# Kernel tuning notes

Hardware: AMD Instinct MI355X
Metric: run time of the kernel (lower is better)

## Reference

```python
import jax, jax.numpy as jnp
import numpy as np

N_NODES = 50000


def _sage_layer(x, edges, W_neigh, W_self, b):
    """HeteroGraphConv(sum) of per-relation DGL SAGEConv(mean).

    x:        [N, F_in] node features (single node type)
    edges:    [R, 2, E] int (src, dst) per relation
    W_neigh:  [R, F_in, F_out], W_self: [R, F_in, F_out], b: [R, F_out]
    returns:  [N, F_out]
    """
    N = x.shape[0]
    R = edges.shape[0]
    out = jnp.zeros((N, W_neigh.shape[-1]), dtype=x.dtype)
    for r in range(R):  # small fixed number of relation types
        src = edges[r, 0]
        dst = edges[r, 1]
        # mean-aggregate neighbor features onto dst
        s = jax.ops.segment_sum(x[src], dst, num_segments=N)          # [N, F_in]
        deg = jax.ops.segment_sum(jnp.ones_like(dst, dtype=x.dtype), dst,
                                  num_segments=N)                     # [N]
        mean = s / jnp.maximum(deg, 1.0)[:, None]                     # zero-deg -> 0
        # SAGEConv(mean): fc_self(h_dst) + fc_neigh(mean_neigh) + bias
        out = out + x @ W_self[r] + mean @ W_neigh[r] + b[r]
    return out


def setup_inputs() -> dict:
    key = jax.random.key(0)
    ks = jax.random.split(key, 10)
    F_in, H, O, R, E = 128, 128, 64, 2, 800000
    scale_in = 1.0 / np.sqrt(F_in)
    scale_h = 1.0 / np.sqrt(H)
    return {
        "x": jax.random.normal(ks[0], (N_NODES, F_in), dtype=jnp.float32),
        "edges": jax.random.randint(ks[1], (R, 2, E), 0, N_NODES, dtype=jnp.int32),
        "neg_edges": jax.random.randint(ks[2], (2, E), 0, N_NODES, dtype=jnp.int32),
        "W_neigh1": jax.random.normal(ks[3], (R, F_in, H), jnp.float32) * scale_in,
        "W_self1": jax.random.normal(ks[4], (R, F_in, H), jnp.float32) * scale_in,
        "b1": jnp.zeros((R, H), jnp.float32),
        "W_neigh2": jax.random.normal(ks[5], (R, H, O), jnp.float32) * scale_h,
        "W_self2": jax.random.normal(ks[6], (R, H, O), jnp.float32) * scale_h,
        "b2": jnp.zeros((R, O), jnp.float32),
    }


def reference(x, edges, neg_edges, W_neigh1, W_self1, b1, W_neigh2, W_self2, b2):
    h = _sage_layer(x, edges, W_neigh1, W_self1, b1)
    h = jax.nn.relu(h)
    h = _sage_layer(h, edges, W_neigh2, W_self2, b2)          # [N, O]
    # HeteroDotProductPredictor: u_dot_v on edges of the scored etype (rel 0)
    pos_score = jnp.sum(h[edges[0, 0]] * h[edges[0, 1]], axis=-1)      # [E]
    neg_score = jnp.sum(h[neg_edges[0]] * h[neg_edges[1]], axis=-1)    # [E_neg]
    return pos_score, neg_score
```

## Files before the change

### kernel.cpp

```cpp
#include <hip/hip_runtime.h>


#define BW 128
#define NBK_MAX 1024
#define EPB 8192

typedef __attribute__((ext_vector_type(8))) short bf16x8;
typedef __attribute__((ext_vector_type(4))) float floatx4;

__device__ __forceinline__ unsigned short f2bf(float f) {
    unsigned u = __float_as_uint(f);
    unsigned r = u + 0x7FFFu + ((u >> 16) & 1u);
    return (unsigned short)(r >> 16);
}
__device__ __forceinline__ unsigned pack2(float a, float b) {
    return (unsigned)f2bf(a) | ((unsigned)f2bf(b) << 16);
}
__device__ __forceinline__ float bflo(unsigned v) { return __uint_as_float(v << 16); }
__device__ __forceinline__ float bfhi(unsigned v) { return __uint_as_float(v & 0xFFFF0000u); }

__global__ __launch_bounds__(256) void
bucket_count_kernel(const int* __restrict__ edges, int* __restrict__ bcnt,
                    int NBK, int E)
{
    __shared__ int cnt[2 * NBK_MAX];
    const int rbT = 2 * NBK;
    const int t = threadIdx.x;
    for (int k = t; k < rbT; k += 256) cnt[k] = 0;
    __syncthreads();
    long long start = (long long)blockIdx.x * EPB;
    long long twoE = 2LL * E;
    for (int u = 0; u < EPB / 256; ++u) {
        long long idx = start + u * 256 + t;
        if (idx < twoE) {
            int r = idx >= E;
            int e = (int)(idx - (long long)r * E);
            int d = edges[(size_t)r * 2 * E + E + e];
            atomicAdd(&cnt[r * NBK + (d >> 7)], 1);
        }
    }
    __syncthreads();
    for (int k = t; k < rbT; k += 256)
        if (cnt[k]) atomicAdd(&bcnt[k], cnt[k]);
}

__global__ __launch_bounds__(1024) void
bucket_scan_kernel(const int* __restrict__ bcnt, int* __restrict__ bko,
                   int rbT, int twoE)
{
    __shared__ int sm[1024];
    int t = threadIdx.x;
    int v = (t < rbT) ? bcnt[t] : 0;
    sm[t] = v;
    __syncthreads();
    for (int s = 1; s < 1024; s <<= 1) {
        int u = (t >= s) ? sm[t - s] : 0;
        __syncthreads();
        sm[t] += u;
        __syncthreads();
    }
    if (t < rbT) bko[t] = sm[t] - v;
    if (t == 0) bko[rbT] = twoE;
}

__global__ __launch_bounds__(256) void
partition_kernel(const int* __restrict__ edges, const int* __restrict__ bko,
                 int* __restrict__ gcur, uint2* __restrict__ staging,
                 int NBK, int E)
{
    __shared__ int cnt[2 * NBK_MAX];
    __shared__ int base[2 * NBK_MAX];
    const int rbT = 2 * NBK;
    const int t = threadIdx.x;
    for (int k = t; k < rbT; k += 256) cnt[k] = 0;
    __syncthreads();
    long long start = (long long)blockIdx.x * EPB;
    long long twoE = 2LL * E;
    for (int u = 0; u < EPB / 256; ++u) {
        long long idx = start + u * 256 + t;
        if (idx < twoE) {
            int r = idx >= E;
            int e = (int)(idx - (long long)r * E);
            int d = edges[(size_t)r * 2 * E + E + e];
            atomicAdd(&cnt[r * NBK + (d >> 7)], 1);
        }
    }
    __syncthreads();
    for (int k = t; k < rbT; k += 256) {
        int c0 = cnt[k];
        if (c0) base[k] = bko[k] + atomicAdd(&gcur[k], c0);
        cnt[k] = 0;
    }
    __syncthreads();
    for (int u = 0; u < EPB / 256; ++u) {
        long long idx = start + u * 256 + t;
        if (idx < twoE) {
            int r = idx >= E;
            int e = (int)(idx - (long long)r * E);
            int s = edges[(size_t)r * 2 * E + e];
            int d = edges[(size_t)r * 2 * E + E + e];
            int rb = r * NBK + (d >> 7);
            int pos = atomicAdd(&cnt[rb], 1);
            staging[(size_t)base[rb] + pos] = make_uint2((unsigned)s, (unsigned)d);
        }
    }
}

__global__ __launch_bounds__(256) void
bucket_csr_kernel(const uint2* __restrict__ staging, const int* __restrict__ bko,
                  int* __restrict__ csr, int* __restrict__ off,
                  int NBK, int N)
{
    __shared__ int hist[BW], excl[BW], cur[BW], sc[BW];
    const int rb = blockIdx.x;
    const int r = rb / NBK;
    const int b = rb % NBK;
    const int node0 = b * BW;
    const int nn = min(BW, N - node0);
    const int cbase = bko[rb];
    const int c = bko[rb + 1] - cbase;
    const int t = threadIdx.x;

    if (t < BW) { hist[t] = 0; cur[t] = 0; }
    __syncthreads();
    for (int k = t; k < c; k += 256)
        atomicAdd(&hist[(int)staging[(size_t)cbase + k].y - node0], 1);
    __syncthreads();
    if (t < BW) sc[t] = hist[t];
    __syncthreads();
    for (int s = 1; s < BW; s <<= 1) {
        int v = (t < BW && t >= s) ? sc[t - s] : 0;
        __syncthreads();
        if (t < BW) sc[t] += v;
        __syncthreads();
    }
    if (t < BW) excl[t] = sc[t] - hist[t];
    if (t < nn) off[(size_t)r * N + node0 + t] = cbase + excl[t];
    __syncthreads();
    for (int k = t; k < c; k += 256) {
        uint2 pr = staging[(size_t)cbase + k];
        int l = (int)pr.y - node0;
        int pos = atomicAdd(&cur[l], 1);
        csr[(size_t)cbase + excl[l] + pos] = (int)pr.x;
    }
}

__global__ void cvt_kernel(const float* __restrict__ in,
                           unsigned short* __restrict__ o, int n4)
{
    int t = blockIdx.x * blockDim.x + threadIdx.x;
    if (t >= n4) return;
    float4 v = ((const float4*)in)[t];
    ushort4 r;
    r.x = f2bf(v.x); r.y = f2bf(v.y); r.z = f2bf(v.z); r.w = f2bf(v.w);
    ((ushort4*)o)[t] = r;
}

__global__ void prep_kernel(const float* __restrict__ Ws1, const float* __restrict__ Wn1,
                            const float* __restrict__ b1,
                            const float* __restrict__ Ws2, const float* __restrict__ Wn2,
                            const float* __restrict__ b2,
                            unsigned short* __restrict__ WT1z, unsigned short* __restrict__ WT1a,
                            unsigned short* __restrict__ WT1b, float* __restrict__ bc1,
                            unsigned short* __restrict__ WT2z, unsigned short* __restrict__ WT2a,
                            unsigned short* __restrict__ WT2b, float* __restrict__ bc2)
{
    int t = blockIdx.x * blockDim.x + threadIdx.x;
    if (t < 16384) {
        int n = t >> 7, k = t & 127;
        int in = k * 128 + n;
        WT1z[t] = f2bf(Ws1[in] + Ws1[16384 + in]);
        WT1a[t] = f2bf(Wn1[in]);
        WT1b[t] = f2bf(Wn1[16384 + in]);
    }
    if (t < 8192) {
        int n = t >> 7, k = t & 127;
        int in = k * 64 + n;
        WT2z[t] = f2bf(Ws2[in] + Ws2[8192 + in]);
        WT2a[t] = f2bf(Wn2[in]);
        WT2b[t] = f2bf(Wn2[8192 + in]);
    }
    if (t < 128) bc1[t] = b1[t] + b1[128 + t];
    if (t < 64)  bc2[t] = b2[t] + b2[64 + t];
}

__global__ __launch_bounds__(256) void
agg1_kernel(const unsigned short* __restrict__ xb,
            const int* __restrict__ csr, const int* __restrict__ off,
            unsigned short* __restrict__ m0, unsigned short* __restrict__ m1,
            int N, int twoE)
{
    int w = blockIdx.x * 4 + (threadIdx.x >> 6);
    int lane = threadIdx.x & 63;
    if (w >= N) return;
    const int col = lane * 2;

    float sx0 = 0.f, sy0 = 0.f, sx1 = 0.f, sy1 = 0.f;
    int o0 = __builtin_amdgcn_readfirstlane(off[w]);
    int o1 = __builtin_amdgcn_readfirstlane(off[w + 1]);
    int d0 = o1 - o0;
    int j = o0;
    for (; j + 7 < o1; j += 8) {
        int s0 = __builtin_amdgcn_readfirstlane(csr[j]);
        int s1 = __builtin_amdgcn_readfirstlane(csr[j + 1]);
        int s2 = __builtin_amdgcn_readfirstlane(csr[j + 2]);
        int s3 = __builtin_amdgcn_readfirstlane(csr[j + 3]);
        int s4 = __builtin_amdgcn_readfirstlane(csr[j + 4]);
        int s5 = __builtin_amdgcn_readfirstlane(csr[j + 5]);
        int s6 = __builtin_amdgcn_readfirstlane(csr[j + 6]);
        int s7 = __builtin_amdgcn_readfirstlane(csr[j + 7]);
        unsigned a0 = *(const unsigned*)(xb + (size_t)s0 * 128 + col);
        unsigned a1 = *(const unsigned*)(xb + (size_t)s1 * 128 + col);
        unsigned a2 = *(const unsigned*)(xb + (size_t)s2 * 128 + col);
        unsigned a3 = *(const unsigned*)(xb + (size_t)s3 * 128 + col);
        unsigned a4 = *(const unsigned*)(xb + (size_t)s4 * 128 + col);
        unsigned a5 = *(const unsigned*)(xb + (size_t)s5 * 128 + col);
        unsigned a6 = *(const unsigned*)(xb + (size_t)s6 * 128 + col);
        unsigned a7 = *(const unsigned*)(xb + (size_t)s7 * 128 + col);
        sx0 += ((bflo(a0) + bflo(a1)) + (bflo(a2) + bflo(a3))) +
               ((bflo(a4) + bflo(a5)) + (bflo(a6) + bflo(a7)));
        sy0 += ((bfhi(a0) + bfhi(a1)) + (bfhi(a2) + bfhi(a3))) +
               ((bfhi(a4) + bfhi(a5)) + (bfhi(a6) + bfhi(a7)));
    }
    for (; j < o1; ++j) {
        int s0 = __builtin_amdgcn_readfirstlane(csr[j]);
        unsigned a = *(const unsigned*)(xb + (size_t)s0 * 128 + col);
        sx0 += bflo(a); sy0 += bfhi(a);
    }
    int p = N + w;
    o0 = __builtin_amdgcn_readfirstlane(off[p]);
    o1 = (p + 1 < 2 * N) ? __builtin_amdgcn_readfirstlane(off[p + 1]) : twoE;
    int d1 = o1 - o0;
    j = o0;
    for (; j + 7 < o1; j += 8) {
        int s0 = __builtin_amdgcn_readfirstlane(csr[j]);
        int s1 = __builtin_amdgcn_readfirstlane(csr[j + 1]);
        int s2 = __builtin_amdgcn_readfirstlane(csr[j + 2]);
        int s3 = __builtin_amdgcn_readfirstlane(csr[j + 3]);
        int s4 = __builtin_amdgcn_readfirstlane(csr[j + 4]);
        int s5 = __builtin_amdgcn_readfirstlane(csr[j + 5]);
        int s6 = __builtin_amdgcn_readfirstlane(csr[j + 6]);
        int s7 = __builtin_amdgcn_readfirstlane(csr[j + 7]);
        unsigned a0 = *(const unsigned*)(xb + (size_t)s0 * 128 + col);
        unsigned a1 = *(const unsigned*)(xb + (size_t)s1 * 128 + col);
        unsigned a2 = *(const unsigned*)(xb + (size_t)s2 * 128 + col);
        unsigned a3 = *(const unsigned*)(xb + (size_t)s3 * 128 + col);
        unsigned a4 = *(const unsigned*)(xb + (size_t)s4 * 128 + col);
        unsigned a5 = *(const unsigned*)(xb + (size_t)s5 * 128 + col);
        unsigned a6 = *(const unsigned*)(xb + (size_t)s6 * 128 + col);
        unsigned a7 = *(const unsigned*)(xb + (size_t)s7 * 128 + col);
        sx1 += ((bflo(a0) + bflo(a1)) + (bflo(a2) + bflo(a3))) +
               ((bflo(a4) + bflo(a5)) + (bflo(a6) + bflo(a7)));
        sy1 += ((bfhi(a0) + bfhi(a1)) + (bfhi(a2) + bfhi(a3))) +
               ((bfhi(a4) + bfhi(a5)) + (bfhi(a6) + bfhi(a7)));
    }
    for (; j < o1; ++j) {
        int s0 = __builtin_amdgcn_readfirstlane(csr[j]);
        unsigned a = *(const unsigned*)(xb + (size_t)s0 * 128 + col);
        sx1 += bflo(a); sy1 += bfhi(a);
    }
    float inv0 = 1.0f / fmaxf((float)d0, 1.0f);
    float inv1 = 1.0f / fmaxf((float)d1, 1.0f);
    *(unsigned*)(m0 + (size_t)w * 128 + col) = pack2(sx0 * inv0, sy0 * inv0);
    *(unsigned*)(m1 + (size_t)w * 128 + col) = pack2(sx1 * inv1, sy1 * inv1);
}

__global__ __launch_bounds__(256) void
gemm1_fused_kernel(const unsigned short* __restrict__ xb,
                   const unsigned short* __restrict__ m0,
                   const unsigned short* __restrict__ m1,
                   const unsigned short* __restrict__ WTz,
                   const unsigned short* __restrict__ WTa,
                   const unsigned short* __restrict__ WTb,
                   const float* __restrict__ bias,
                   unsigned short* __restrict__ h1b, int N)
{
    __shared__ float eb[64][129];

    const int tid = threadIdx.x;
    const int wave = tid >> 6;
    const int lane = tid & 63;
    const int m = lane & 15;
    const int quad = lane >> 4;

    floatx4 acc[8];
    const floatx4 z4 = {0.f, 0.f, 0.f, 0.f};
#pragma unroll
    for (int t = 0; t < 8; ++t) acc[t] = z4;

    int arow = blockIdx.x * 64 + wave * 16 + m;
    if (arow >= N) arow = N - 1;
    const size_t abase = (size_t)arow * 128 + quad * 8;

#pragma unroll
    for (int s = 0; s < 4; ++s) {
        bf16x8 ax = *(const bf16x8*)(xb + abase + s * 32);
        bf16x8 a0 = *(const bf16x8*)(m0 + abase + s * 32);
        bf16x8 a1 = *(const bf16x8*)(m1 + abase + s * 32);
#pragma unroll
        for (int t = 0; t < 8; ++t) {
            const size_t bo = (size_t)(t * 16 + m) * 128 + s * 32 + quad * 8;
            acc[t] = __builtin_amdgcn_mfma_f32_16x16x32_bf16(
                ax, *(const bf16x8*)(WTz + bo), acc[t], 0, 0, 0);
            acc[t] = __builtin_amdgcn_mfma_f32_16x16x32_bf16(
                a0, *(const bf16x8*)(WTa + bo), acc[t], 0, 0, 0);
            acc[t] = __builtin_amdgcn_mfma_f32_16x16x32_bf16(
                a1, *(const bf16x8*)(WTb + bo), acc[t], 0, 0, 0);
        }
    }

#pragma unroll
    for (int t = 0; t < 8; ++t)
#pragma unroll
        for (int i = 0; i < 4; ++i)
            eb[wave * 16 + quad * 4 + i][t * 16 + m] = acc[t][i];
    __syncthreads();

#pragma unroll
    for (int j = 0; j < 4; ++j) {
        int lr = wave * 16 + j * 4 + quad;
        int grow = blockIdx.x * 64 + lr;
        if (grow < N) {
#pragma unroll
            for (int i = 0; i < 2; ++i) {
                int c0 = (i * 16 + m) * 4;
                float v0 = fmaxf(eb[lr][c0 + 0] + bias[c0 + 0], 0.0f);
                float v1 = fmaxf(eb[lr][c0 + 1] + bias[c0 + 1], 0.0f);
                float v2 = fmaxf(eb[lr][c0 + 2] + bias[c0 + 2], 0.0f);
                float v3 = fmaxf(eb[lr][c0 + 3] + bias[c0 + 3], 0.0f);
                ushort4 u;
                u.x = f2bf(v0); u.y = f2bf(v1); u.z = f2bf(v2); u.w = f2bf(v3);
                *(ushort4*)(h1b + (size_t)grow * 128 + c0) = u;
            }
        }
    }
}

template<int BN>
__global__ __launch_bounds__(256) void
gemm_mfma_kernel(const unsigned short* __restrict__ Ab,
                 const unsigned short* __restrict__ WTz,
                 const unsigned short* __restrict__ WTa,
                 const unsigned short* __restrict__ WTb,
                 const float* __restrict__ bias,
                 float* __restrict__ zf,
                 unsigned short* __restrict__ ya, unsigned short* __restrict__ yb,
                 int N)
{
    constexpr int NT = BN / 16;
    __shared__ float eb[64][BN + 1];

    const int tid = threadIdx.x;
    const int wave = tid >> 6;
    const int lane = tid & 63;
    const int m = lane & 15;
    const int quad = lane >> 4;
    const int sel = blockIdx.y;
    const unsigned short* WT = (sel == 0) ? WTz : ((sel == 1) ? WTa : WTb);

    floatx4 acc[NT];
    const floatx4 z4 = {0.f, 0.f, 0.f, 0.f};
#pragma unroll
    for (int t = 0; t < NT; ++t) acc[t] = z4;

    int arow = blockIdx.x * 64 + wave * 16 + m;
    if (arow >= N) arow = N - 1;
    const unsigned short* aptr = Ab + (size_t)arow * 128 + quad * 8;

#pragma unroll
    for (int s = 0; s < 4; ++s) {
        bf16x8 a = *(const bf16x8*)(aptr + s * 32);
#pragma unroll
        for (int t = 0; t < NT; ++t) {
            bf16x8 b = *(const bf16x8*)(WT + (size_t)(t * 16 + m) * 128 + s * 32 + quad * 8);
            acc[t] = __builtin_amdgcn_mfma_f32_16x16x32_bf16(a, b, acc[t], 0, 0, 0);
        }
    }

#pragma unroll
    for (int t = 0; t < NT; ++t)
#pragma unroll
        for (int i = 0; i < 4; ++i)
            eb[wave * 16 + quad * 4 + i][t * 16 + m] = acc[t][i];
    __syncthreads();

#pragma unroll
    for (int j = 0; j < 4; ++j) {
        int lr = wave * 16 + j * 4 + quad;
        int grow = blockIdx.x * 64 + lr;
        if (grow < N) {
#pragma unroll
            for (int i = 0; i < BN / 64; ++i) {
                int c0 = (i * 16 + m) * 4;
                float v0 = eb[lr][c0 + 0], v1 = eb[lr][c0 + 1];
                float v2 = eb[lr][c0 + 2], v3 = eb[lr][c0 + 3];
                if (sel == 0) {
                    float4 o;
                    o.x = v0 + bias[c0 + 0];
                    o.y = v1 + bias[c0 + 1];
                    o.z = v2 + bias[c0 + 2];
                    o.w = v3 + bias[c0 + 3];
                    *(float4*)(zf + (size_t)grow * BN + c0) = o;
                } else {
                    unsigned short* ob = (sel == 1) ? ya : yb;
                    ushort4 u;
                    u.x = f2bf(v0); u.y = f2bf(v1); u.z = f2bf(v2); u.w = f2bf(v3);
                    *(ushort4*)(ob + (size_t)grow * BN + c0) = u;
                }
            }
        }
    }
}

__global__ __launch_bounds__(256) void
agg2_kernel(const unsigned short* __restrict__ t0,
            const unsigned short* __restrict__ t1,
            const float* __restrict__ z2,
            const int* __restrict__ csr, const int* __restrict__ off,
            unsigned short* __restrict__ h2b, int N, int twoE)
{
    int w = blockIdx.x * 4 + (threadIdx.x >> 6);
    int lane = threadIdx.x & 63;
    if (w >= N) return;
    const int half = lane >> 5;
    const int col = (lane & 31) * 2;

    float sx0 = 0.f, sy0 = 0.f, sx1 = 0.f, sy1 = 0.f;
    int o0 = __builtin_amdgcn_readfirstlane(off[w]);
    int o1 = __builtin_amdgcn_readfirstlane(off[w + 1]);
    int d0 = o1 - o0;
    int j = o0 + half;
    for (; j + 6 < o1; j += 8) {
        int s0 = csr[j], s1 = csr[j + 2], s2 = csr[j + 4], s3 = csr[j + 6];
        unsigned a0 = *(const unsigned*)(t0 + (size_t)s0 * 64 + col);
        unsigned a1 = *(const unsigned*)(t0 + (size_t)s1 * 64 + col);
        unsigned a2 = *(const unsigned*)(t0 + (size_t)s2 * 64 + col);
        unsigned a3 = *(const unsigned*)(t0 + (size_t)s3 * 64 + col);
        sx0 += (bflo(a0) + bflo(a1)) + (bflo(a2) + bflo(a3));
        sy0 += (bfhi(a0) + bfhi(a1)) + (bfhi(a2) + bfhi(a3));
    }
    for (; j < o1; j += 2) {
        unsigned a = *(const unsigned*)(t0 + (size_t)csr[j] * 64 + col);
        sx0 += bflo(a); sy0 += bfhi(a);
    }
    int p = N + w;
    o0 = __builtin_amdgcn_readfirstlane(off[p]);
    o1 = (p + 1 < 2 * N) ? __builtin_amdgcn_readfirstlane(off[p + 1]) : twoE;
    int d1 = o1 - o0;
    j = o0 + half;
    for (; j + 6 < o1; j += 8) {
        int s0 = csr[j], s1 = csr[j + 2], s2 = csr[j + 4], s3 = csr[j + 6];
        unsigned a0 = *(const unsigned*)(t1 + (size_t)s0 * 64 + col);
        unsigned a1 = *(const unsigned*)(t1 + (size_t)s1 * 64 + col);
        unsigned a2 = *(const unsigned*)(t1 + (size_t)s2 * 64 + col);
        unsigned a3 = *(const unsigned*)(t1 + (size_t)s3 * 64 + col);
        sx1 += (bflo(a0) + bflo(a1)) + (bflo(a2) + bflo(a3));
        sy1 += (bfhi(a0) + bfhi(a1)) + (bfhi(a2) + bfhi(a3));
    }
    for (; j < o1; j += 2) {
        unsigned a = *(const unsigned*)(t1 + (size_t)csr[j] * 64 + col);
        sx1 += bflo(a); sy1 += bfhi(a);
    }
    sx0 += __shfl_xor(sx0, 32);
    sy0 += __shfl_xor(sy0, 32);
    sx1 += __shfl_xor(sx1, 32);
    sy1 += __shfl_xor(sy1, 32);
    if (half == 0) {
        float inv0 = 1.0f / fmaxf((float)d0, 1.0f);
        float inv1 = 1.0f / fmaxf((float)d1, 1.0f);
        float2 z = *(const float2*)(z2 + (size_t)w * 64 + col);
        float hx = z.x + sx0 * inv0 + sx1 * inv1;
        float hy = z.y + sy0 * inv0 + sy1 * inv1;
        *(unsigned*)(h2b + (size_t)w * 64 + col) = pack2(hx, hy);
    }
}

__global__ __launch_bounds__(256) void
score_kernel(const unsigned short* __restrict__ h,
             const int* __restrict__ edges, const int* __restrict__ neg,
             float* __restrict__ out, int E, int En)
{
    int t = blockIdx.x * blockDim.x + threadIdx.x;
    int e = t >> 3;
    int c = t & 7;
    if (e >= E + En) return;
    int sI, dI, oI;
    if (e < E) { sI = edges[e]; dI = edges[E + e]; oI = e; }
    else { int en = e - E; sI = neg[en]; dI = neg[En + en]; oI = E + en; }
    uint4 va = *(const uint4*)(h + (size_t)sI * 64 + c * 8);
    uint4 vb = *(const uint4*)(h + (size_t)dI * 64 + c * 8);
    float s = 0.0f;
    s = fmaf(bflo(va.x), bflo(vb.x), s);
    s = fmaf(bfhi(va.x), bfhi(vb.x), s);
    s = fmaf(bflo(va.y), bflo(vb.y), s);
    s = fmaf(bfhi(va.y), bfhi(vb.y), s);
    s = fmaf(bflo(va.z), bflo(vb.z), s);
    s = fmaf(bfhi(va.z), bfhi(vb.z), s);
    s = fmaf(bflo(va.w), bflo(vb.w), s);
    s = fmaf(bfhi(va.w), bfhi(vb.w), s);
    s += __shfl_xor(s, 1);
    s += __shfl_xor(s, 2);
    s += __shfl_xor(s, 4);
    if (c == 0) out[oI] = s;
}

extern "C" void kernel_launch(void* const* d_in, const int* in_sizes, int n_in,
                              void* d_out, int out_size, void* d_ws, size_t ws_size,
                              hipStream_t stream)
{
    const float* x     = (const float*)d_in[0];
    const int*   edges = (const int*)d_in[1];
    const int*   neg   = (const int*)d_in[2];
    const float* Wn1   = (const float*)d_in[3];
    const float* Ws1   = (const float*)d_in[4];
    const float* b1    = (const float*)d_in[5];
    const float* Wn2   = (const float*)d_in[6];
    const float* Ws2   = (const float*)d_in[7];
    const float* b2    = (const float*)d_in[8];
    float* out = (float*)d_out;

    const int Fin = 128, R = 2;
    const int N  = in_sizes[0] / Fin;
    const int E  = in_sizes[1] / (R * 2);
    const int En = in_sizes[2] / 2;
    const int twoE = 2 * E;
    const int NBK = (N + BW - 1) / BW;
    const int rbT = 2 * NBK;

    const size_t nb128 = (size_t)N * 128 * sizeof(unsigned short);
    char* p = (char*)d_ws;

    uint2* staging = (uint2*)p;
    float* z2      = (float*)p;
    {
        size_t r0 = (size_t)twoE * sizeof(uint2);
        size_t r1 = (size_t)N * 64 * sizeof(float);
        p += (r0 > r1 ? r0 : r1);
    }
    unsigned short* m0  = (unsigned short*)p; p += nb128;
    unsigned short* m1  = (unsigned short*)p; p += nb128;
    unsigned short* xb  = (unsigned short*)p; p += nb128;
    unsigned short* h1b = (unsigned short*)p; p += nb128;
    unsigned short* WT1z = (unsigned short*)p; p += 16384 * 2;
    unsigned short* WT1a = (unsigned short*)p; p += 16384 * 2;
    unsigned short* WT1b = (unsigned short*)p; p += 16384 * 2;
    unsigned short* WT2z = (unsigned short*)p; p += 8192 * 2;
    unsigned short* WT2a = (unsigned short*)p; p += 8192 * 2;
    unsigned short* WT2b = (unsigned short*)p; p += 8192 * 2;
    float* bc1 = (float*)p; p += 128 * sizeof(float);
    float* bc2 = (float*)p; p += 64 * sizeof(float);
    int* bcnt = (int*)p; p += (size_t)2 * NBK_MAX * sizeof(int);
    int* gcur = (int*)p; p += (size_t)2 * NBK_MAX * sizeof(int);
    int* bko  = (int*)p; p += ((size_t)2 * NBK_MAX + 1) * sizeof(int);
    int* off  = (int*)p; p += (size_t)2 * N * sizeof(int);
    int* csr  = (int*)p;

    unsigned short* t0  = m0;
    unsigned short* t1  = m0 + (size_t)N * 64;
    unsigned short* h2b = m1;

    const int BS = 256;
    const int edge_blocks = (twoE + EPB - 1) / EPB;
    const int gx = (N + 63) / 64;

    hipMemsetAsync(bcnt, 0, (size_t)4 * NBK_MAX * sizeof(int), stream);
    bucket_count_kernel<<<edge_blocks, BS, 0, stream>>>(edges, bcnt, NBK, E);
    bucket_scan_kernel<<<1, 1024, 0, stream>>>(bcnt, bko, rbT, twoE);
    partition_kernel<<<edge_blocks, BS, 0, stream>>>(edges, bko, gcur, staging, NBK, E);
    bucket_csr_kernel<<<rbT, BS, 0, stream>>>(staging, bko, csr, off, NBK, N);

    cvt_kernel<<<(N * 32 + BS - 1) / BS, BS, 0, stream>>>(x, xb, N * 32);
    prep_kernel<<<(16384 + BS - 1) / BS, BS, 0, stream>>>(
        Ws1, Wn1, b1, Ws2, Wn2, b2,
        WT1z, WT1a, WT1b, bc1, WT2z, WT2a, WT2b, bc2);

    agg1_kernel<<<(N + 3) / 4, BS, 0, stream>>>(xb, csr, off, m0, m1, N, twoE);
    gemm1_fused_kernel<<<gx, BS, 0, stream>>>(xb, m0, m1, WT1z, WT1a, WT1b,
                                              bc1, h1b, N);

    {
        dim3 g(gx, 3);
        gemm_mfma_kernel<64><<<g, BS, 0, stream>>>(h1b, WT2z, WT2a, WT2b, bc2,
                                                   z2, t0, t1, N);
    }
    agg2_kernel<<<(N + 3) / 4, BS, 0, stream>>>(t0, t1, z2, csr, off, h2b, N, twoE);

    score_kernel<<<((E + En) * 8 + BS - 1) / BS, BS, 0, stream>>>(
        h2b, edges, neg, out, E, En);
}
```

Before: 383.7 us.

## Split gather rows across half-waves with wider loads; fuse layer-2 GEMM outputs

agg1 now has each half-wave gather a different neighbor row with 8-byte loads, merging the halves by shuffle. agg2 now uses quarter-wave groups of four rows each with 8-byte loads. Both aim to put more independent memory requests in flight per wave. The three-way blockIdx.y layer-2 GEMM is merged into one kernel that reloads the A tile once and computes all three outputs, at the cost of more accumulator registers and extra shared-memory round trips.

```diff
diff --git a/kernel.cpp b/kernel.cpp
--- a/kernel.cpp
+++ b/kernel.cpp
@@ -18,6 +18,7 @@
 }
 __device__ __forceinline__ float bflo(unsigned v) { return __uint_as_float(v << 16); }
 __device__ __forceinline__ float bfhi(unsigned v) { return __uint_as_float(v & 0xFFFF0000u); }
+#define RFL(x) __builtin_amdgcn_readfirstlane(x)
 
 __global__ __launch_bounds__(256) void
 bucket_count_kernel(const int* __restrict__ edges, int* __restrict__ bcnt,
@@ -193,76 +194,119 @@
     int w = blockIdx.x * 4 + (threadIdx.x >> 6);
     int lane = threadIdx.x & 63;
     if (w >= N) return;
-    const int col = lane * 2;
-
-    float sx0 = 0.f, sy0 = 0.f, sx1 = 0.f, sy1 = 0.f;
-    int o0 = __builtin_amdgcn_readfirstlane(off[w]);
-    int o1 = __builtin_amdgcn_readfirstlane(off[w + 1]);
+    const int half = lane >> 5;
+    const int col = (lane & 31) * 4;
+    const unsigned short* xc = xb + col;
+
+    float a0 = 0.f, a1 = 0.f, a2 = 0.f, a3 = 0.f;
+    float b0 = 0.f, b1 = 0.f, b2 = 0.f, b3 = 0.f;
+
+    int o0 = RFL(off[w]);
+    int o1 = RFL(off[w + 1]);
     int d0 = o1 - o0;
     int j = o0;
+    for (; j + 15 < o1; j += 16) {
+        int cc[16];
+#pragma unroll
+        for (int k = 0; k < 16; ++k) cc[k] = RFL(csr[j + k]);
+#pragma unroll
+        for (int k = 0; k < 8; ++k) {
+            int row = half ? cc[2 * k + 1] : cc[2 * k];
+            uint2 v = *(const uint2*)(xc + (size_t)row * 128);
+            a0 += bflo(v.x); a1 += bfhi(v.x);
+            a2 += bflo(v.y); a3 += bfhi(v.y);
+        }
+    }
     for (; j + 7 < o1; j += 8) {
-        int s0 = __builtin_amdgcn_readfirstlane(csr[j]);
-        int s1 = __builtin_amdgcn_readfirstlane(csr[j + 1]);
-        int s2 = __builtin_amdgcn_readfirstlane(csr[j + 2]);
-        int s3 = __builtin_amdgcn_readfirstlane(csr[j + 3]);
-        int s4 = __builtin_amdgcn_readfirstlane(csr[j + 4]);
-        int s5 = __builtin_amdgcn_readfirstlane(csr[j + 5]);
-        int s6 = __builtin_amdgcn_readfirstlane(csr[j + 6]);
-        int s7 = __builtin_amdgcn_readfirstlane(csr[j + 7]);
-        unsigned a0 = *(const unsigned*)(xb + (size_t)s0 * 128 + col);
-        unsigned a1 = *(const unsigned*)(xb + (size_t)s1 * 128 + col);
-        unsigned a2 = *(const unsigned*)(xb + (size_t)s2 * 128 + col);
-        unsigned a3 = *(const unsigned*)(xb + (size_t)s3 * 128 + col);
-        unsigned a4 = *(const unsigned*)(xb + (size_t)s4 * 128 + col);
-        unsigned a5 = *(const unsigned*)(xb + (size_t)s5 * 128 + col);
-        unsigned a6 = *(const unsigned*)(xb + (size_t)s6 * 128 + col);
-        unsigned a7 = *(const unsigned*)(xb + (size_t)s7 * 128 + col);
-        sx0 += ((bflo(a0) + bflo(a1)) + (bflo(a2) + bflo(a3))) +
-               ((bflo(a4) + bflo(a5)) + (bflo(a6) + bflo(a7)));
-        sy0 += ((bfhi(a0) + bfhi(a1)) + (bfhi(a2) + bfhi(a3))) +
-               ((bfhi(a4) + bfhi(a5)) + (bfhi(a6) + bfhi(a7)));
-    }
-    for (; j < o1; ++j) {
-        int s0 = __builtin_amdgcn_readfirstlane(csr[j]);
-        unsigned a = *(const unsigned*)(xb + (size_t)s0 * 128 + col);
-        sx0 += bflo(a); sy0 += bfhi(a);
-    }
+        int cc[8];
+#pragma unroll
+        for (int k = 0; k < 8; ++k) cc[k] = RFL(csr[j + k]);
+#pragma unroll
+        for (int k = 0; k < 4; ++k) {
+            int row = half ? cc[2 * k + 1] : cc[2 * k];
+            uint2 v = *(const uint2*)(xc + (size_t)row * 128);
+            a0 += bflo(v.x); a1 += bfhi(v.x);
+            a2 += bflo(v.y); a3 += bfhi(v.y);
+        }
+    }
+    for (; j + 1 < o1; j += 2) {
+        int rlo = RFL(csr[j]);
+        int rhi = RFL(csr[j + 1]);
+        int row = half ? rhi : rlo;
+        uint2 v = *(const uint2*)(xc + (size_t)row * 128);
+        a0 += bflo(v.x); a1 += bfhi(v.x);
+        a2 += bflo(v.y); a3 += bfhi(v.y);
+    }
+    if (j < o1) {
+        int row = RFL(csr[j]);
+        if (half == 0) {
+            uint2 v = *(const uint2*)(xc + (size_t)row * 128);
+            a0 += bflo(v.x); a1 += bfhi(v.x);
+            a2 += bflo(v.y); a3 += bfhi(v.y);
+        }
+    }
+
     int p = N + w;
-    o0 = __builtin_amdgcn_readfirstlane(off[p]);
-    o1 = (p + 1 < 2 * N) ? __builtin_amdgcn_readfirstlane(off[p + 1]) : twoE;
+    o0 = RFL(off[p]);
+    o1 = (p + 1 < 2 * N) ? RFL(off[p + 1]) : twoE;
     int d1 = o1 - o0;
     j = o0;
+    for (; j + 15 < o1; j += 16) {
+        int cc[16];
+#pragma unroll
+        for (int k = 0; k < 16; ++k) cc[k] = RFL(csr[j + k]);
+#pragma unroll
+        for (int k = 0; k < 8; ++k) {
+            int row = half ? cc[2 * k + 1] : cc[2 * k];
+            uint2 v = *(const uint2*)(xc + (size_t)row * 128);
+            b0 += bflo(v.x); b1 += bfhi(v.x);
+            b2 += bflo(v.y); b3 += bfhi(v.y);
+        }
+    }
     for (; j + 7 < o1; j += 8) {
-        int s0 = __builtin_amdgcn_readfirstlane(csr[j]);
-        int s1 = __builtin_amdgcn_readfirstlane(csr[j + 1]);
-        int s2 = __builtin_amdgcn_readfirstlane(csr[j + 2]);
-        int s3 = __builtin_amdgcn_readfirstlane(csr[j + 3]);
-        int s4 = __builtin_amdgcn_readfirstlane(csr[j + 4]);
-        int s5 = __builtin_amdgcn_readfirstlane(csr[j + 5]);
-        int s6 = __builtin_amdgcn_readfirstlane(csr[j + 6]);
-        int s7 = __builtin_amdgcn_readfirstlane(csr[j + 7]);
-        unsigned a0 = *(const unsigned*)(xb + (size_t)s0 * 128 + col);
-        unsigned a1 = *(const unsigned*)(xb + (size_t)s1 * 128 + col);
-        unsigned a2 = *(const unsigned*)(xb + (size_t)s2 * 128 + col);
-        unsigned a3 = *(const unsigned*)(xb + (size_t)s3 * 128 + col);
-        unsigned a4 = *(const unsigned*)(xb + (size_t)s4 * 128 + col);
-        unsigned a5 = *(const unsigned*)(xb + (size_t)s5 * 128 + col);
-        unsigned a6 = *(const unsigned*)(xb + (size_t)s6 * 128 + col);
-        unsigned a7 = *(const unsigned*)(xb + (size_t)s7 * 128 + col);
-        sx1 += ((bflo(a0) + bflo(a1)) + (bflo(a2) + bflo(a3))) +
-               ((bflo(a4) + bflo(a5)) + (bflo(a6) + bflo(a7)));
-        sy1 += ((bfhi(a0) + bfhi(a1)) + (bfhi(a2) + bfhi(a3))) +
-               ((bfhi(a4) + bfhi(a5)) + (bfhi(a6) + bfhi(a7)));
-    }
-    for (; j < o1; ++j) {
-        int s0 = __builtin_amdgcn_readfirstlane(csr[j]);
-        unsigned a = *(const unsigned*)(xb + (size_t)s0 * 128 + col);
-        sx1 += bflo(a); sy1 += bfhi(a);
-    }
-    float inv0 = 1.0f / fmaxf((float)d0, 1.0f);
-    float inv1 = 1.0f / fmaxf((float)d1, 1.0f);
-    *(unsigned*)(m0 + (size_t)w * 128 + col) = pack2(sx0 * inv0, sy0 * inv0);
-    *(unsigned*)(m1 + (size_t)w * 128 + col) = pack2(sx1 * inv1, sy1 * inv1);
+        int cc[8];
+#pragma unroll
+        for (int k = 0; k < 8; ++k) cc[k] = RFL(csr[j + k]);
+#pragma unroll
+        for (int k = 0; k < 4; ++k) {
+            int row = half ? cc[2 * k + 1] : cc[2 * k];
+            uint2 v = *(const uint2*)(xc + (size_t)row * 128);
+            b0 += bflo(v.x); b1 += bfhi(v.x);
+            b2 += bflo(v.y); b3 += bfhi(v.y);
+        }
+    }
+    for (; j + 1 < o1; j += 2) {
+        int rlo = RFL(csr[j]);
+        int rhi = RFL(csr[j + 1]);
+        int row = half ? rhi : rlo;
+        uint2 v = *(const uint2*)(xc + (size_t)row * 128);
+        b0 += bflo(v.x); b1 += bfhi(v.x);
+        b2 += bflo(v.y); b3 += bfhi(v.y);
+    }
+    if (j < o1) {
+        int row = RFL(csr[j]);
+        if (half == 0) {
+            uint2 v = *(const uint2*)(xc + (size_t)row * 128);
+            b0 += bflo(v.x); b1 += bfhi(v.x);
+            b2 += bflo(v.y); b3 += bfhi(v.y);
+        }
+    }
+
+    a0 += __shfl_xor(a0, 32); a1 += __shfl_xor(a1, 32);
+    a2 += __shfl_xor(a2, 32); a3 += __shfl_xor(a3, 32);
+    b0 += __shfl_xor(b0, 32); b1 += __shfl_xor(b1, 32);
+    b2 += __shfl_xor(b2, 32); b3 += __shfl_xor(b3, 32);
+    if (half == 0) {
+        float inv0 = 1.0f / fmaxf((float)d0, 1.0f);
+        float inv1 = 1.0f / fmaxf((float)d1, 1.0f);
+        uint2 u0, u1;
+        u0.x = pack2(a0 * inv0, a1 * inv0);
+        u0.y = pack2(a2 * inv0, a3 * inv0);
+        u1.x = pack2(b0 * inv1, b1 * inv1);
+        u1.y = pack2(b2 * inv1, b3 * inv1);
+        *(uint2*)(m0 + (size_t)w * 128 + col) = u0;
+        *(uint2*)(m1 + (size_t)w * 128 + col) = u1;
+    }
 }
 
 __global__ __launch_bounds__(256) void
@@ -336,32 +380,28 @@
     }
 }
 
-template<int BN>
 __global__ __launch_bounds__(256) void
-gemm_mfma_kernel(const unsigned short* __restrict__ Ab,
-                 const unsigned short* __restrict__ WTz,
-                 const unsigned short* __restrict__ WTa,
-                 const unsigned short* __restrict__ WTb,
-                 const float* __restrict__ bias,
-                 float* __restrict__ zf,
-                 unsigned short* __restrict__ ya, unsigned short* __restrict__ yb,
-                 int N)
-{
-    constexpr int NT = BN / 16;
-    __shared__ float eb[64][BN + 1];
+gemm2_fused_kernel(const unsigned short* __restrict__ Ab,
+                   const unsigned short* __restrict__ WTz,
+                   const unsigned short* __restrict__ WTa,
+                   const unsigned short* __restrict__ WTb,
+                   const float* __restrict__ bias,
+                   float* __restrict__ zf,
+                   unsigned short* __restrict__ ya, unsigned short* __restrict__ yb,
+                   int N)
+{
+    __shared__ float eb[64][65];
 
     const int tid = threadIdx.x;
     const int wave = tid >> 6;
     const int lane = tid & 63;
     const int m = lane & 15;
     const int quad = lane >> 4;
-    const int sel = blockIdx.y;
-    const unsigned short* WT = (sel == 0) ? WTz : ((sel == 1) ? WTa : WTb);
-
-    floatx4 acc[NT];
+
+    floatx4 accz[4], acca[4], accb[4];
     const floatx4 z4 = {0.f, 0.f, 0.f, 0.f};
 #pragma unroll
-    for (int t = 0; t < NT; ++t) acc[t] = z4;
+    for (int t = 0; t < 4; ++t) { accz[t] = z4; acca[t] = z4; accb[t] = z4; }
 
     int arow = blockIdx.x * 64 + wave * 16 + m;
     if (arow >= N) arow = N - 1;
@@ -371,45 +411,80 @@
     for (int s = 0; s < 4; ++s) {
         bf16x8 a = *(const bf16x8*)(aptr + s * 32);
 #pragma unroll
-        for (int t = 0; t < NT; ++t) {
-            bf16x8 b = *(const bf16x8*)(WT + (size_t)(t * 16 + m) * 128 + s * 32 + quad * 8);
-            acc[t] = __builtin_amdgcn_mfma_f32_16x16x32_bf16(a, b, acc[t], 0, 0, 0);
-        }
-    }
-
-#pragma unroll
-    for (int t = 0; t < NT; ++t)
+        for (int t = 0; t < 4; ++t) {
+            const size_t bo = (size_t)(t * 16 + m) * 128 + s * 32 + quad * 8;
+            accz[t] = __builtin_amdgcn_mfma_f32_16x16x32_bf16(
+                a, *(const bf16x8*)(WTz + bo), accz[t], 0, 0, 0);
+            acca[t] = __builtin_amdgcn_mfma_f32_16x16x32_bf16(
+                a, *(const bf16x8*)(WTa + bo), acca[t], 0, 0, 0);
+            accb[t] = __builtin_amdgcn_mfma_f32_16x16x32_bf16(
+                a, *(const bf16x8*)(WTb + bo), accb[t], 0, 0, 0);
+        }
+    }
+
+    const int grow = blockIdx.x * 64 + wave * 16;
+
+#pragma unroll
+    for (int t = 0; t < 4; ++t)
 #pragma unroll
         for (int i = 0; i < 4; ++i)
-            eb[wave * 16 + quad * 4 + i][t * 16 + m] = acc[t][i];
-    __syncthreads();
-
+            eb[wave * 16 + quad * 4 + i][t * 16 + m] = accz[t][i];
+    __syncthreads();
 #pragma unroll
     for (int j = 0; j < 4; ++j) {
         int lr = wave * 16 + j * 4 + quad;
-        int grow = blockIdx.x * 64 + lr;
-        if (grow < N) {
-#pragma unroll
-            for (int i = 0; i < BN / 64; ++i) {
-                int c0 = (i * 16 + m) * 4;
-                float v0 = eb[lr][c0 + 0], v1 = eb[lr][c0 + 1];
-                float v2 = eb[lr][c0 + 2], v3 = eb[lr][c0 + 3];
-                if (sel == 0) {
-                    float4 o;
-                    o.x = v0 + bias[c0 + 0];
-                    o.y = v1 + bias[c0 + 1];
-                    o.z = v2 + bias[c0 + 2];
-                    o.w = v3 + bias[c0 + 3];
-                    *(float4*)(zf + (size_t)grow * BN + c0) = o;
-                } else {
-                    unsigned short* ob = (sel == 1) ? ya : yb;
-                    ushort4 u;
-                    u.x = f2bf(v0); u.y = f2bf(v1); u.z = f2bf(v2); u.w = f2bf(v3);
-                    *(ushort4*)(ob + (size_t)grow * BN + c0) = u;
-                }
-            }
-        }
-    }
+        int gr = blockIdx.x * 64 + lr;
+        if (gr < N) {
+            int c0 = m * 4;
+            float4 o;
+            o.x = eb[lr][c0 + 0] + bias[c0 + 0];
+            o.y = eb[lr][c0 + 1] + bias[c0 + 1];
+            o.z = eb[lr][c0 + 2] + bias[c0 + 2];
+            o.w = eb[lr][c0 + 3] + bias[c0 + 3];
+            *(float4*)(zf + (size_t)gr * 64 + c0) = o;
+        }
+    }
+    __syncthreads();
+
+#pragma unroll
+    for (int t = 0; t < 4; ++t)
+#pragma unroll
+        for (int i = 0; i < 4; ++i)
+            eb[wave * 16 + quad * 4 + i][t * 16 + m] = acca[t][i];
+    __syncthreads();
+#pragma unroll
+    for (int j = 0; j < 4; ++j) {
+        int lr = wave * 16 + j * 4 + quad;
+        int gr = blockIdx.x * 64 + lr;
+        if (gr < N) {
+            int c0 = m * 4;
+            ushort4 u;
+            u.x = f2bf(eb[lr][c0 + 0]); u.y = f2bf(eb[lr][c0 + 1]);
+            u.z = f2bf(eb[lr][c0 + 2]); u.w = f2bf(eb[lr][c0 + 3]);
+            *(ushort4*)(ya + (size_t)gr * 64 + c0) = u;
+        }
+    }
+    __syncthreads();
+
+#pragma unroll
+    for (int t = 0; t < 4; ++t)
+#pragma unroll
+        for (int i = 0; i < 4; ++i)
+            eb[wave * 16 + quad * 4 + i][t * 16 + m] = accb[t][i];
+    __syncthreads();
+#pragma unroll
+    for (int j = 0; j < 4; ++j) {
+        int lr = wave * 16 + j * 4 + quad;
+        int gr = blockIdx.x * 64 + lr;
+        if (gr < N) {
+            int c0 = m * 4;
+            ushort4 u;
+            u.x = f2bf(eb[lr][c0 + 0]); u.y = f2bf(eb[lr][c0 + 1]);
+            u.z = f2bf(eb[lr][c0 + 2]); u.w = f2bf(eb[lr][c0 + 3]);
+            *(ushort4*)(yb + (size_t)gr * 64 + c0) = u;
+        }
+    }
+    (void)grow;
 }
 
 __global__ __launch_bounds__(256) void
@@ -422,56 +497,111 @@
     int w = blockIdx.x * 4 + (threadIdx.x >> 6);
     int lane = threadIdx.x & 63;
     if (w >= N) return;
-    const int half = lane >> 5;
-    const int col = (lane & 31) * 2;
-
-    float sx0 = 0.f, sy0 = 0.f, sx1 = 0.f, sy1 = 0.f;
-    int o0 = __builtin_amdgcn_readfirstlane(off[w]);
-    int o1 = __builtin_amdgcn_readfirstlane(off[w + 1]);
+    const int q = lane >> 4;
+    const int col = (lane & 15) * 4;
+    const unsigned short* t0c = t0 + col;
+    const unsigned short* t1c = t1 + col;
+
+    float a0 = 0.f, a1 = 0.f, a2 = 0.f, a3 = 0.f;
+    float b0 = 0.f, b1 = 0.f, b2 = 0.f, b3 = 0.f;
+
+    int o0 = RFL(off[w]);
+    int o1 = RFL(off[w + 1]);
     int d0 = o1 - o0;
-    int j = o0 + half;
-    for (; j + 6 < o1; j += 8) {
-        int s0 = csr[j], s1 = csr[j + 2], s2 = csr[j + 4], s3 = csr[j + 6];
-        unsigned a0 = *(const unsigned*)(t0 + (size_t)s0 * 64 + col);
-        unsigned a1 = *(const unsigned*)(t0 + (size_t)s1 * 64 + col);
-        unsigned a2 = *(const unsigned*)(t0 + (size_t)s2 * 64 + col);
-        unsigned a3 = *(const unsigned*)(t0 + (size_t)s3 * 64 + col);
-        sx0 += (bflo(a0) + bflo(a1)) + (bflo(a2) + bflo(a3));
-        sy0 += (bfhi(a0) + bfhi(a1)) + (bfhi(a2) + bfhi(a3));
-    }
-    for (; j < o1; j += 2) {
-        unsigned a = *(const unsigned*)(t0 + (size_t)csr[j] * 64 + col);
-        sx0 += bflo(a); sy0 += bfhi(a);
-    }
+    int j = o0;
+    for (; j + 15 < o1; j += 16) {
+        int cc[16];
+#pragma unroll
+        for (int k = 0; k < 16; ++k) cc[k] = RFL(csr[j + k]);
+#pragma unroll
+        for (int k = 0; k < 4; ++k) {
+            int r01 = (q & 1) ? cc[4 * k + 1] : cc[4 * k];
+            int r23 = (q & 1) ? cc[4 * k + 3] : cc[4 * k + 2];
+            int row = (q & 2) ? r23 : r01;
+            uint2 v = *(const uint2*)(t0c + (size_t)row * 64);
+            a0 += bflo(v.x); a1 += bfhi(v.x);
+            a2 += bflo(v.y); a3 += bfhi(v.y);
+        }
+    }
+    for (; j + 3 < o1; j += 4) {
+        int c0 = RFL(csr[j]), c1 = RFL(csr[j + 1]);
+        int c2 = RFL(csr[j + 2]), c3 = RFL(csr[j + 3]);
+        int r01 = (q & 1) ? c1 : c0;
+        int r23 = (q & 1) ? c3 : c2;
+        int row = (q & 2) ? r23 : r01;
+        uint2 v = *(const uint2*)(t0c + (size_t)row * 64);
+        a0 += bflo(v.x); a1 += bfhi(v.x);
+        a2 += bflo(v.y); a3 += bfhi(v.y);
+    }
+    if (j < o1) {
+        int rem = o1 - j;
+        if (q < rem) {
+            int row = csr[j + q];
+            uint2 v = *(const uint2*)(t0c + (size_t)row * 64);
+            a0 += bflo(v.x); a1 += bfhi(v.x);
+            a2 += bflo(v.y); a3 += bfhi(v.y);
+        }
+    }
+
     int p = N + w;
-    o0 = __builtin_amdgcn_readfirstlane(off[p]);
-    o1 = (p + 1 < 2 * N) ? __builtin_amdgcn_readfirstlane(off[p + 1]) : twoE;
+    o0 = RFL(off[p]);
+    o1 = (p + 1 < 2 * N) ? RFL(off[p + 1]) : twoE;
     int d1 = o1 - o0;
-    j = o0 + half;
-    for (; j + 6 < o1; j += 8) {
-        int s0 = csr[j], s1 = csr[j + 2], s2 = csr[j + 4], s3 = csr[j + 6];
-        unsigned a0 = *(const unsigned*)(t1 + (size_t)s0 * 64 + col);
-        unsigned a1 = *(const unsigned*)(t1 + (size_t)s1 * 64 + col);
-        unsigned a2 = *(const unsigned*)(t1 + (size_t)s2 * 64 + col);
-        unsigned a3 = *(const unsigned*)(t1 + (size_t)s3 * 64 + col);
-        sx1 += (bflo(a0) + bflo(a1)) + (bflo(a2) + bflo(a3));
-        sy1 += (bfhi(a0) + bfhi(a1)) + (bfhi(a2) + bfhi(a3));
-    }
-    for (; j < o1; j += 2) {
-        unsigned a = *(const unsigned*)(t1 + (size_t)csr[j] * 64 + col);
-        sx1 += bflo(a); sy1 += bfhi(a);
-    }
-    sx0 += __shfl_xor(sx0, 32);
-    sy0 += __shfl_xor(sy0, 32);
-    sx1 += __shfl_xor(sx1, 32);
-    sy1 += __shfl_xor(sy1, 32);
-    if (half == 0) {
+    j = o0;
+    for (; j + 15 < o1; j += 16) {
+        int cc[16];
+#pragma unroll
+        for (int k = 0; k < 16; ++k) cc[k] = RFL(csr[j + k]);
+#pragma unroll
+        for (int k = 0; k < 4; ++k) {
+            int r01 = (q & 1) ? cc[4 * k + 1] : cc[4 * k];
+            int r23 = (q & 1) ? cc[4 * k + 3] : cc[4 * k + 2];
+            int row = (q & 2) ? r23 : r01;
+            uint2 v = *(const uint2*)(t1c + (size_t)row * 64);
+            b0 += bflo(v.x); b1 += bfhi(v.x);
+            b2 += bflo(v.y); b3 += bfhi(v.y);
+        }
+    }
+    for (; j + 3 < o1; j += 4) {
+        int c0 = RFL(csr[j]), c1 = RFL(csr[j + 1]);
+        int c2 = RFL(csr[j + 2]), c3 = RFL(csr[j + 3]);
+        int r01 = (q & 1) ? c1 : c0;
+        int r23 = (q & 1) ? c3 : c2;
+        int row = (q & 2) ? r23 : r01;
+        uint2 v = *(const uint2*)(t1c + (size_t)row * 64);
+        b0 += bflo(v.x); b1 += bfhi(v.x);
+        b2 += bflo(v.y); b3 += bfhi(v.y);
+    }
+    if (j < o1) {
+        int rem = o1 - j;
+        if (q < rem) {
+            int row = csr[j + q];
+            uint2 v = *(const uint2*)(t1c + (size_t)row * 64);
+            b0 += bflo(v.x); b1 += bfhi(v.x);
+            b2 += bflo(v.y); b3 += bfhi(v.y);
+        }
+    }
+
+    a0 += __shfl_xor(a0, 16); a1 += __shfl_xor(a1, 16);
+    a2 += __shfl_xor(a2, 16); a3 += __shfl_xor(a3, 16);
+    b0 += __shfl_xor(b0, 16); b1 += __shfl_xor(b1, 16);
+    b2 += __shfl_xor(b2, 16); b3 += __shfl_xor(b3, 16);
+    a0 += __shfl_xor(a0, 32); a1 += __shfl_xor(a1, 32);
+    a2 += __shfl_xor(a2, 32); a3 += __shfl_xor(a3, 32);
+    b0 += __shfl_xor(b0, 32); b1 += __shfl_xor(b1, 32);
+    b2 += __shfl_xor(b2, 32); b3 += __shfl_xor(b3, 32);
+    if (q == 0) {
         float inv0 = 1.0f / fmaxf((float)d0, 1.0f);
         float inv1 = 1.0f / fmaxf((float)d1, 1.0f);
-        float2 z = *(const float2*)(z2 + (size_t)w * 64 + col);
-        float hx = z.x + sx0 * inv0 + sx1 * inv1;
-        float hy = z.y + sy0 * inv0 + sy1 * inv1;
-        *(unsigned*)(h2b + (size_t)w * 64 + col) = pack2(hx, hy);
+        float4 z = *(const float4*)(z2 + (size_t)w * 64 + col);
+        float h0 = z.x + a0 * inv0 + b0 * inv1;
+        float h1 = z.y + a1 * inv0 + b1 * inv1;
+        float h2 = z.z + a2 * inv0 + b2 * inv1;
+        float h3 = z.w + a3 * inv0 + b3 * inv1;
+        uint2 u;
+        u.x = pack2(h0, h1);
+        u.y = pack2(h2, h3);
+        *(uint2*)(h2b + (size_t)w * 64 + col) = u;
     }
 }
 
@@ -578,11 +708,8 @@
     gemm1_fused_kernel<<<gx, BS, 0, stream>>>(xb, m0, m1, WT1z, WT1a, WT1b,
                                               bc1, h1b, N);
 
-    {
-        dim3 g(gx, 3);
-        gemm_mfma_kernel<64><<<g, BS, 0, stream>>>(h1b, WT2z, WT2a, WT2b, bc2,
-                                                   z2, t0, t1, N);
-    }
+    gemm2_fused_kernel<<<gx, BS, 0, stream>>>(h1b, WT2z, WT2a, WT2b, bc2,
+                                              z2, t0, t1, N);
     agg2_kernel<<<(N + 3) / 4, BS, 0, stream>>>(t0, t1, z2, csr, off, h2b, N, twoE);
 
     score_kernel<<<((E + En) * 8 + BS - 1) / BS, BS, 0, stream>>>(
```

Measured after the change: 440.5 us. 14.8% more time.
